# Performance work log

Hardware: AMD Instinct MI355X
Metric: run time of the kernel (lower is better)

## Reference

```python
import jax, jax.numpy as jnp
import numpy as np

H = 32          # query heads
KV = 8          # kv heads
DH = 64         # head dim
WINDOW = 1024   # sliding window
BASE = 10000.0  # rope base


def _rope(x, pos):
    """Interleaved RoPE as in RotaryEmbedding.apply. x: (B,H,T,Dh), pos: (T,)."""
    inv = 1.0 / (BASE ** (jnp.arange(0, DH, 2, dtype=jnp.float32) / DH))  # (Dh/2,)
    freqs = pos.astype(jnp.float32)[:, None] * inv[None, :]               # (T, Dh/2)
    cos = jnp.cos(freqs)[None, None].astype(x.dtype)
    sin = jnp.sin(freqs)[None, None].astype(x.dtype)
    x1, x2 = x[..., ::2], x[..., 1::2]
    o1 = x1 * cos - x2 * sin
    o2 = x1 * sin + x2 * cos
    return jnp.stack([o1, o2], axis=-1).reshape(x.shape)


def setup_inputs() -> dict:
    key = jax.random.key(0)
    ks = jax.random.split(key, 5)
    B, T, D, Tc = 2, 4096, 2048, 4096
    x = jax.random.normal(ks[0], (B, T, D), jnp.float32)
    k_cache = jax.random.normal(ks[1], (B, KV, Tc, DH), jnp.float32)
    v_cache = jax.random.normal(ks[2], (B, KV, Tc, DH), jnp.float32)
    Wq = jax.random.normal(ks[3], (D, D), jnp.float32) * 0.02
    Wo = jax.random.normal(ks[4], (D, D), jnp.float32) * 0.02
    return {"x": x, "k_cache": k_cache, "v_cache": v_cache, "Wq": Wq, "Wo": Wo}


def reference(x, k_cache, v_cache, Wq, Wo):
    """AttnLayer.forward, role='follower', local=True, return_attn=False, eval mode."""
    B, T, D = x.shape
    rep = H // KV
    # q projection: nn.Linear(d, H*Dh, bias=False) -> x @ W.T
    q = (x @ Wq.T).reshape(B, T, H, DH).transpose(0, 2, 1, 3)  # (B,H,T,Dh)
    Tc = k_cache.shape[2]
    pos_q = jnp.arange(Tc - T, Tc)
    q = _rope(q, pos_q)
    # GQA: KV -> H head replication (repeat_interleave along head dim)
    k = jnp.repeat(k_cache, rep, axis=1)  # (B,H,Tc,Dh)
    v = jnp.repeat(v_cache, rep, axis=1)
    # sliding-window slice: keep last `window` keys
    w = min(WINDOW, Tc)
    k = k[:, :, Tc - w:, :]  # (B,H,Tk,Dh)
    v = v[:, :, Tc - w:, :]
    Tk = w
    scale = 1.0 / np.sqrt(DH).astype(np.float32)
    scores = jnp.einsum('bhtd,bhsd->bhts', q, k) * scale  # (B,H,T,Tk)
    # torch SDPA is_causal with L != S uses a TOP-LEFT aligned tril mask: j <= i
    causal = jnp.arange(Tk)[None, :] <= jnp.arange(T)[:, None]  # (T,Tk)
    scores = jnp.where(causal[None, None], scores, -jnp.inf)
    attn = jax.nn.softmax(scores, axis=-1)
    out = jnp.einsum('bhts,bhsd->bhtd', attn, v)
    out = out.transpose(0, 2, 1, 3).reshape(B, T, H * DH)
    return out @ Wo.T
```

## Files before the change

### kernel.cpp

```cpp
#include <hip/hip_runtime.h>
#include <math.h>

typedef __attribute__((ext_vector_type(8))) short short8;
typedef __attribute__((ext_vector_type(4))) float floatx4;
typedef __attribute__((ext_vector_type(4))) unsigned int uintx4;
typedef __attribute__((ext_vector_type(2))) unsigned int uintx2;

#define MFMA16(a, b, c) __builtin_amdgcn_mfma_f32_16x16x32_bf16((a), (b), (c), 0, 0, 0)

#define QSCALE 0.18033688011112042f

__device__ __forceinline__ unsigned short f2bf(float x) {
    unsigned int u = __float_as_uint(x);
    u += 0x7fffu + ((u >> 16) & 1u);
    return (unsigned short)(u >> 16);
}

__device__ __forceinline__ short8 lds8(const unsigned short* p) {
    return *reinterpret_cast<const short8*>(p);
}

__device__ __forceinline__ void g2l16(const unsigned short* g, unsigned short* l) {
    __builtin_amdgcn_global_load_lds(
        (const __attribute__((address_space(1))) unsigned int*)g,
        (__attribute__((address_space(3))) unsigned int*)l,
        16, 0, 0);
}

__device__ __forceinline__ unsigned int cvtpk(float a, float b) {
    unsigned int r;
    asm("v_cvt_pk_bf16_f32 %0, %1, %2" : "=v"(r) : "v"(a), "v"(b));
    return r;
}

__device__ __forceinline__ void pl32swap(unsigned int& a, unsigned int& b) {
    asm("v_permlane32_swap_b32 %0, %1" : "+v"(a), "+v"(b));
}

__device__ __forceinline__ void pl16swap(unsigned int& a, unsigned int& b) {
    asm("v_permlane16_swap_b32 %0, %1" : "+v"(a), "+v"(b));
}

__global__ void cvt_bf16(const float* __restrict__ src, unsigned short* __restrict__ dst, int n4) {
    int i = blockIdx.x * blockDim.x + threadIdx.x;
    if (i >= n4) return;
    float4 v = reinterpret_cast<const float4*>(src)[i];
    ushort4 o;
    o.x = f2bf(v.x); o.y = f2bf(v.y); o.z = f2bf(v.z); o.w = f2bf(v.w);
    reinterpret_cast<ushort4*>(dst)[i] = o;
}

__global__ void prep_k(const float* __restrict__ kc, unsigned short* __restrict__ Kw) {
    int i = blockIdx.x * blockDim.x + threadIdx.x;
    int d4  = (i & 15) * 4;
    int s   = (i >> 4) & 1023;
    int bkv = i >> 14;
    size_t src = ((size_t)bkv * 4096 + 3072 + s) * 64 + d4;
    float4 kv = *reinterpret_cast<const float4*>(kc + src);
    ushort4 ko;
    ko.x = f2bf(kv.x); ko.y = f2bf(kv.y); ko.z = f2bf(kv.z); ko.w = f2bf(kv.w);
    *reinterpret_cast<ushort4*>(Kw + ((size_t)bkv * 1024 + s) * 64 + d4) = ko;
}

__global__ void prep_v(const float* __restrict__ vc, unsigned short* __restrict__ Vt) {
    __shared__ unsigned short tl[64][72];
    const int bkv = blockIdx.x >> 4;
    const int s0  = (blockIdx.x & 15) * 64;
    const int t   = threadIdx.x;
    const int sl  = t >> 2;
    const int dq  = (t & 3) * 16;
    const float* src = vc + ((size_t)bkv * 4096 + 3072 + s0 + sl) * 64 + dq;
    float4 v0 = reinterpret_cast<const float4*>(src)[0];
    float4 v1 = reinterpret_cast<const float4*>(src)[1];
    float4 v2 = reinterpret_cast<const float4*>(src)[2];
    float4 v3 = reinterpret_cast<const float4*>(src)[3];
    tl[dq +  0][sl] = f2bf(v0.x); tl[dq +  1][sl] = f2bf(v0.y);
    tl[dq +  2][sl] = f2bf(v0.z); tl[dq +  3][sl] = f2bf(v0.w);
    tl[dq +  4][sl] = f2bf(v1.x); tl[dq +  5][sl] = f2bf(v1.y);
    tl[dq +  6][sl] = f2bf(v1.z); tl[dq +  7][sl] = f2bf(v1.w);
    tl[dq +  8][sl] = f2bf(v2.x); tl[dq +  9][sl] = f2bf(v2.y);
    tl[dq + 10][sl] = f2bf(v2.z); tl[dq + 11][sl] = f2bf(v2.w);
    tl[dq + 12][sl] = f2bf(v3.x); tl[dq + 13][sl] = f2bf(v3.y);
    tl[dq + 14][sl] = f2bf(v3.z); tl[dq + 15][sl] = f2bf(v3.w);
    __syncthreads();
    const int dl = t >> 2;
    const int sc = (t & 3) * 16;
    unsigned short* dst = Vt + ((size_t)bkv * 64 + dl) * 1024 + s0 + sc;
    short8 x0 = *reinterpret_cast<const short8*>(&tl[dl][sc]);
    short8 x1 = *reinterpret_cast<const short8*>(&tl[dl][sc + 8]);
    *reinterpret_cast<short8*>(dst)     = x0;
    *reinterpret_cast<short8*>(dst + 8) = x1;
}

template <int EPI>
__global__ __launch_bounds__(256)
void gemm_bt(const unsigned short* __restrict__ A,
             const unsigned short* __restrict__ Bt,
             float* __restrict__ Cf,
             unsigned short* __restrict__ Cb) {
    constexpr int K = 2048;
    __shared__ unsigned short As[128 * 32];
    __shared__ unsigned short Bs[128 * 32];
    __shared__ float2 tab[EPI == 0 ? 128 * 33 : 1];

    const int tid  = threadIdx.x;
    const int lane = tid & 63;
    const int l15  = lane & 15;
    const int quad = lane >> 4;
    const int wid  = tid >> 6;
    const int wm   = (wid & 1) * 64;
    const int wn   = (wid >> 1) * 64;

    const int bn = blockIdx.x & 15;
    const int bm = blockIdx.x >> 4;

    if (EPI == 0) {
        const int t0 = (bm & 31) * 128;
        for (int e = tid; e < 4096; e += 256) {
            int tl = e >> 5, d2 = e & 31;
            float f = (float)(t0 + tl) * exp2f(-(float)d2 * 0.41524101186092f);
            float sn, cs; __sincosf(f, &sn, &cs);
            tab[tl * 33 + d2] = make_float2(cs, sn);
        }
    }

    const int row0 = tid >> 2;
    const int kc8  = (tid & 3) * 8;
    const unsigned short* Ag0 = A  + (size_t)(bm * 128 + row0) * K + kc8;
    const unsigned short* Ag1 = Ag0 + (size_t)64 * K;
    const unsigned short* Bg0 = Bt + (size_t)(bn * 128 + row0) * K + kc8;
    const unsigned short* Bg1 = Bg0 + (size_t)64 * K;
    unsigned short* AsW0 = As + wid * 512;
    unsigned short* AsW1 = As + 2048 + wid * 512;
    unsigned short* BsW0 = Bs + wid * 512;
    unsigned short* BsW1 = Bs + 2048 + wid * 512;

    floatx4 c00 = {0,0,0,0}, c01 = {0,0,0,0}, c02 = {0,0,0,0}, c03 = {0,0,0,0};
    floatx4 c10 = {0,0,0,0}, c11 = {0,0,0,0}, c12 = {0,0,0,0}, c13 = {0,0,0,0};
    floatx4 c20 = {0,0,0,0}, c21 = {0,0,0,0}, c22 = {0,0,0,0}, c23 = {0,0,0,0};
    floatx4 c30 = {0,0,0,0}, c31 = {0,0,0,0}, c32 = {0,0,0,0}, c33 = {0,0,0,0};

    for (int k0 = 0; k0 < K; k0 += 32) {
        __syncthreads();
        g2l16(Ag0 + k0, AsW0);
        g2l16(Ag1 + k0, AsW1);
        g2l16(Bg0 + k0, BsW0);
        g2l16(Bg1 + k0, BsW1);
        __syncthreads();

        short8 a0 = lds8(&As[(wm +  0 + l15) * 32 + quad * 8]);
        short8 a1 = lds8(&As[(wm + 16 + l15) * 32 + quad * 8]);
        short8 a2 = lds8(&As[(wm + 32 + l15) * 32 + quad * 8]);
        short8 a3 = lds8(&As[(wm + 48 + l15) * 32 + quad * 8]);
        short8 b0 = lds8(&Bs[(wn +  0 + l15) * 32 + quad * 8]);
        short8 b1 = lds8(&Bs[(wn + 16 + l15) * 32 + quad * 8]);
        short8 b2 = lds8(&Bs[(wn + 32 + l15) * 32 + quad * 8]);
        short8 b3 = lds8(&Bs[(wn + 48 + l15) * 32 + quad * 8]);

        c00 = MFMA16(a0, b0, c00); c01 = MFMA16(a0, b1, c01);
        c02 = MFMA16(a0, b2, c02); c03 = MFMA16(a0, b3, c03);
        c10 = MFMA16(a1, b0, c10); c11 = MFMA16(a1, b1, c11);
        c12 = MFMA16(a1, b2, c12); c13 = MFMA16(a1, b3, c13);
        c20 = MFMA16(a2, b0, c20); c21 = MFMA16(a2, b1, c21);
        c22 = MFMA16(a2, b2, c22); c23 = MFMA16(a2, b3, c23);
        c30 = MFMA16(a3, b0, c30); c31 = MFMA16(a3, b1, c31);
        c32 = MFMA16(a3, b2, c32); c33 = MFMA16(a3, b3, c33);
    }

#define EPI_TILE(i, j, C) do {                                                  \
    _Pragma("unroll")                                                           \
    for (int r = 0; r < 4; ++r) {                                               \
        int row = bm * 128 + wm + (i) * 16 + quad * 4 + r;                      \
        int col = bn * 128 + wn + (j) * 16 + l15;                               \
        float v = (C)[r];                                                       \
        if (EPI == 0) {                                                         \
            float p = __shfl_xor(v, 1);                                         \
            int t = row & 4095, b = row >> 12;                                  \
            int hh = col >> 6, d = col & 63;                                    \
            int tl = wm + (i) * 16 + quad * 4 + r;                              \
            float2 cspair = tab[tl * 33 + (d >> 1)];                            \
            float o = (d & 1) ? (p * cspair.y + v * cspair.x)                   \
                              : (v * cspair.x - p * cspair.y);                  \
            o *= QSCALE;                                                        \
            float po = __shfl_xor(o, 1);                                        \
            if (!(lane & 1)) {                                                  \
                unsigned int pk = (unsigned int)f2bf(o) |                       \
                                  ((unsigned int)f2bf(po) << 16);               \
                *reinterpret_cast<unsigned int*>(                               \
                    Cb + ((size_t)((b * 32 + hh) * 4096 + t)) * 64 + d) = pk;   \
            }                                                                   \
        } else {                                                                \
            Cf[(size_t)row * 2048 + col] = v;                                   \
        }                                                                       \
    }                                                                           \
} while (0)

    EPI_TILE(0, 0, c00); EPI_TILE(0, 1, c01); EPI_TILE(0, 2, c02); EPI_TILE(0, 3, c03);
    EPI_TILE(1, 0, c10); EPI_TILE(1, 1, c11); EPI_TILE(1, 2, c12); EPI_TILE(1, 3, c13);
    EPI_TILE(2, 0, c20); EPI_TILE(2, 1, c21); EPI_TILE(2, 2, c22); EPI_TILE(2, 3, c23);
    EPI_TILE(3, 0, c30); EPI_TILE(3, 1, c31); EPI_TILE(3, 2, c32); EPI_TILE(3, 3, c33);
#undef EPI_TILE
}

__global__ __launch_bounds__(256, 5)
void attn(const unsigned short* __restrict__ Q,
          const unsigned short* __restrict__ Kw,
          const unsigned short* __restrict__ Vt,
          unsigned short* __restrict__ O) {
    const int blk   = blockIdx.x;
    const int qtile = blk & 63;
    const int bh    = blk >> 6;
    const int h     = bh & 31;
    const int b     = bh >> 5;
    const int kvh   = h >> 2;

    const int tid  = threadIdx.x;
    const int lane = tid & 63;
    const int l15  = lane & 15;
    const int quad = lane >> 4;
    const int wid  = tid >> 6;
    const int qt0  = qtile * 64 + wid * 16;

    const unsigned short* Qp = Q  + ((size_t)bh * 4096 + qt0) * 64;
    const unsigned short* Kp = Kw + (size_t)(b * 8 + kvh) * 1024 * 64;
    const unsigned short* Vp = Vt + (size_t)(b * 8 + kvh) * 64 * 1024;

    __shared__ unsigned short Ks[2][4096];
    __shared__ unsigned short Vs[2][4096];

    short8 qa0 = lds8(&Qp[l15 * 64 + quad * 8]);
    short8 qa1 = lds8(&Qp[l15 * 64 + 32 + quad * 8]);

    const unsigned short* gK = Kp + (size_t)(wid * 16 + l15) * 64 + quad * 8;
    const unsigned short* gV = Vp + (size_t)(wid * 16 + l15) * 1024 + quad * 8;

    const int ntiles = (qtile < 15 ? qtile + 1 : 16);
    const int nkW    = (qt0 + 16 < 1024) ? qt0 + 16 : 1024;
    const bool diag  = (qtile < 16);

    g2l16(gK,      &Ks[0][wid * 1024]);
    g2l16(gK + 32, &Ks[0][wid * 1024 + 512]);
    g2l16(gV,      &Vs[0][wid * 1024]);
    g2l16(gV + 32, &Vs[0][wid * 1024 + 512]);

    floatx4 o0 = {0,0,0,0}, o1 = {0,0,0,0}, o2 = {0,0,0,0}, o3 = {0,0,0,0};
    float Lq = 0.f;
    float m = -INFINITY;

    for (int it = 0; it < ntiles; ++it) {
        __syncthreads();
        const int cur = it & 1;
        if (it + 1 < ntiles) {
            const int nxt = cur ^ 1;
            const unsigned short* gKn = gK + (it + 1) * 4096;
            const unsigned short* gVn = gV + (it + 1) * 64;
            g2l16(gKn,      &Ks[nxt][wid * 1024]);
            g2l16(gKn + 32, &Ks[nxt][wid * 1024 + 512]);
            g2l16(gVn,      &Vs[nxt][wid * 1024]);
            g2l16(gVn + 32, &Vs[nxt][wid * 1024 + 512]);
        }
        const int s0 = it << 6;
        const unsigned short* Kc = Ks[cur];
        const unsigned short* Vc = Vs[cur];

        floatx4 sS[4];
#pragma unroll
        for (int c = 0; c < 4; ++c) {
            floatx4 z = {0, 0, 0, 0};
            z = MFMA16(lds8(Kc + c * 1024 + lane * 8), qa0, z);
            z = MFMA16(lds8(Kc + c * 1024 + 512 + lane * 8), qa1, z);
            sS[c] = z;
        }

        const bool last = (it == ntiles - 1);
        bool skipHi = false;
        if (last && diag) {
#pragma unroll
            for (int c = 0; c < 4; ++c)
#pragma unroll
                for (int r = 0; r < 4; ++r)
                    if (s0 + c * 16 + quad * 4 + r > qt0 + l15) sS[c][r] = -INFINITY;
            skipHi = (nkW - s0 <= 32);
        }

        float t0 = fmaxf(fmaxf(sS[0][0], sS[0][1]), fmaxf(sS[0][2], sS[0][3]));
        float t1 = fmaxf(fmaxf(sS[1][0], sS[1][1]), fmaxf(sS[1][2], sS[1][3]));
        float t2 = fmaxf(fmaxf(sS[2][0], sS[2][1]), fmaxf(sS[2][2], sS[2][3]));
        float t3 = fmaxf(fmaxf(sS[3][0], sS[3][1]), fmaxf(sS[3][2], sS[3][3]));
        float mx = fmaxf(fmaxf(t0, t1), fmaxf(t2, t3));
        mx = fmaxf(mx, __shfl_xor(mx, 16));
        mx = fmaxf(mx, __shfl_xor(mx, 32));

        if (!__all(mx <= m + 8.0f)) {
            const float mn = fmaxf(m, mx);
            const float alpha = exp2f(m - mn);
            m = mn;
            o0 *= alpha; o1 *= alpha; o2 *= alpha; o3 *= alpha;
            Lq *= alpha;
        }

        float p[4][4];
#pragma unroll
        for (int c = 0; c < 4; ++c)
#pragma unroll
            for (int r = 0; r < 4; ++r) p[c][r] = exp2f(sS[c][r] - m);
        Lq += ((p[0][0] + p[0][1] + p[0][2] + p[0][3]) + (p[1][0] + p[1][1] + p[1][2] + p[1][3]))
            + ((p[2][0] + p[2][1] + p[2][2] + p[2][3]) + (p[3][0] + p[3][1] + p[3][2] + p[3][3]));

        unsigned int a0 = cvtpk(p[0][0], p[0][1]);
        unsigned int a1 = cvtpk(p[0][2], p[0][3]);
        unsigned int a2 = cvtpk(p[1][0], p[1][1]);
        unsigned int a3 = cvtpk(p[1][2], p[1][3]);
        pl32swap(a0, a2); pl32swap(a1, a3);
        pl16swap(a0, a2); pl16swap(a1, a3);
        uintx4 tlo = {a0, a1, a2, a3};
        short8 pa_lo = __builtin_bit_cast(short8, tlo);

        o0 = MFMA16(lds8(Vc + 0 * 512 + lane * 8), pa_lo, o0);
        o1 = MFMA16(lds8(Vc + 2 * 512 + lane * 8), pa_lo, o1);
        o2 = MFMA16(lds8(Vc + 4 * 512 + lane * 8), pa_lo, o2);
        o3 = MFMA16(lds8(Vc + 6 * 512 + lane * 8), pa_lo, o3);
        if (!skipHi) {
            unsigned int b0 = cvtpk(p[2][0], p[2][1]);
            unsigned int b1 = cvtpk(p[2][2], p[2][3]);
            unsigned int b2 = cvtpk(p[3][0], p[3][1]);
            unsigned int b3 = cvtpk(p[3][2], p[3][3]);
            pl32swap(b0, b2); pl32swap(b1, b3);
            pl16swap(b0, b2); pl16swap(b1, b3);
            uintx4 thi = {b0, b1, b2, b3};
            short8 pa_hi = __builtin_bit_cast(short8, thi);
            o0 = MFMA16(lds8(Vc + 1 * 512 + lane * 8), pa_hi, o0);
            o1 = MFMA16(lds8(Vc + 3 * 512 + lane * 8), pa_hi, o1);
            o2 = MFMA16(lds8(Vc + 5 * 512 + lane * 8), pa_hi, o2);
            o3 = MFMA16(lds8(Vc + 7 * 512 + lane * 8), pa_hi, o3);
        }
    }

    Lq += __shfl_xor(Lq, 16);
    Lq += __shfl_xor(Lq, 32);
    const float inv = 1.f / Lq;

    unsigned short* Op = O + (size_t)b * 4096 * 2048 + (size_t)(qt0 + l15) * 2048
                           + h * 64 + quad * 4;
    uintx2 w0, w1, w2, w3;
    w0.x = cvtpk(o0[0] * inv, o0[1] * inv); w0.y = cvtpk(o0[2] * inv, o0[3] * inv);
    w1.x = cvtpk(o1[0] * inv, o1[1] * inv); w1.y = cvtpk(o1[2] * inv, o1[3] * inv);
    w2.x = cvtpk(o2[0] * inv, o2[1] * inv); w2.y = cvtpk(o2[2] * inv, o2[3] * inv);
    w3.x = cvtpk(o3[0] * inv, o3[1] * inv); w3.y = cvtpk(o3[2] * inv, o3[3] * inv);
    *reinterpret_cast<uintx2*>(Op)      = w0;
    *reinterpret_cast<uintx2*>(Op + 16) = w1;
    *reinterpret_cast<uintx2*>(Op + 32) = w2;
    *reinterpret_cast<uintx2*>(Op + 48) = w3;
}

extern "C" void kernel_launch(void* const* d_in, const int* in_sizes, int n_in,
                              void* d_out, int out_size, void* d_ws, size_t ws_size,
                              hipStream_t stream) {
    const float* x  = (const float*)d_in[0];
    const float* kc = (const float*)d_in[1];
    const float* vc = (const float*)d_in[2];
    const float* Wq = (const float*)d_in[3];
    const float* Wo = (const float*)d_in[4];
    float* out = (float*)d_out;

    char* ws = (char*)d_ws;
    unsigned short* Xb  = (unsigned short*)(ws);
    unsigned short* Qb  = (unsigned short*)(ws + 33554432);
    unsigned short* Wqb = (unsigned short*)(ws + 67108864);
    unsigned short* Wob = (unsigned short*)(ws + 75497472);
    unsigned short* Kwb = (unsigned short*)(ws + 83886080);
    unsigned short* Vtb = (unsigned short*)(ws + 85983232);

    cvt_bf16<<<16384, 256, 0, stream>>>(x,  Xb,  4194304);
    cvt_bf16<<<4096,  256, 0, stream>>>(Wq, Wqb, 1048576);
    cvt_bf16<<<4096,  256, 0, stream>>>(Wo, Wob, 1048576);
    prep_k<<<1024, 256, 0, stream>>>(kc, Kwb);
    prep_v<<<256, 256, 0, stream>>>(vc, Vtb);

    gemm_bt<0><<<1024, 256, 0, stream>>>(Xb, Wqb, nullptr, Qb);
    attn<<<4096, 256, 0, stream>>>(Qb, Kwb, Vtb, Xb);
    gemm_bt<1><<<1024, 256, 0, stream>>>(Xb, Wob, out, nullptr);
}
```

Measured before the change: 511.3 us.

## Use 8-wave attention blocks covering 128 queries to share K/V tiles

The attention kernel now launches half as many blocks, each with 512 threads covering 128 query rows instead of 64. Each K/V LDS tile is loaded cooperatively by eight waves, so every global K/V tile is fetched once per 128 queries rather than once per 64, which halves global and LDS fill traffic. Waves whose causal window ends early skip the compute for tiles beyond their own range but still take part in loading and barriers. The cost is some idle waves on diagonal blocks, and the launch bound of 512 threads at 8 waves per SIMD tightens the register budget.

```diff
diff --git a/kernel.cpp b/kernel.cpp
--- a/kernel.cpp
+++ b/kernel.cpp
@@ -202,24 +202,24 @@
 #undef EPI_TILE
 }
 
-__global__ __launch_bounds__(256, 5)
+__global__ __launch_bounds__(512, 8)
 void attn(const unsigned short* __restrict__ Q,
           const unsigned short* __restrict__ Kw,
           const unsigned short* __restrict__ Vt,
           unsigned short* __restrict__ O) {
-    const int blk   = blockIdx.x;
-    const int qtile = blk & 63;
-    const int bh    = blk >> 6;
-    const int h     = bh & 31;
-    const int b     = bh >> 5;
-    const int kvh   = h >> 2;
+    const int blk  = blockIdx.x;
+    const int qblk = blk & 31;
+    const int bh   = blk >> 5;
+    const int h    = bh & 31;
+    const int b    = bh >> 5;
+    const int kvh  = h >> 2;
 
     const int tid  = threadIdx.x;
     const int lane = tid & 63;
     const int l15  = lane & 15;
     const int quad = lane >> 4;
     const int wid  = tid >> 6;
-    const int qt0  = qtile * 64 + wid * 16;
+    const int qt0  = qblk * 128 + wid * 16;
 
     const unsigned short* Qp = Q  + ((size_t)bh * 4096 + qt0) * 64;
     const unsigned short* Kp = Kw + (size_t)(b * 8 + kvh) * 1024 * 64;
@@ -231,17 +231,22 @@
     short8 qa0 = lds8(&Qp[l15 * 64 + quad * 8]);
     short8 qa1 = lds8(&Qp[l15 * 64 + 32 + quad * 8]);
 
-    const unsigned short* gK = Kp + (size_t)(wid * 16 + l15) * 64 + quad * 8;
-    const unsigned short* gV = Vp + (size_t)(wid * 16 + l15) * 1024 + quad * 8;
-
-    const int ntiles = (qtile < 15 ? qtile + 1 : 16);
+    const unsigned short* gK = Kp + (size_t)((wid >> 1) * 16 + l15) * 64
+                                  + (wid & 1) * 32 + quad * 8;
+    const unsigned short* gV = Vp + (size_t)((wid >> 1) * 16 + l15) * 1024
+                                  + (wid & 1) * 32 + quad * 8;
+    unsigned short* sK0 = &Ks[0][wid * 512];
+    unsigned short* sK1 = &Ks[1][wid * 512];
+    unsigned short* sV0 = &Vs[0][wid * 512];
+    unsigned short* sV1 = &Vs[1][wid * 512];
+
+    const int ntiles = (qblk < 7 ? 2 * qblk + 2 : 16);
     const int nkW    = (qt0 + 16 < 1024) ? qt0 + 16 : 1024;
-    const bool diag  = (qtile < 16);
-
-    g2l16(gK,      &Ks[0][wid * 1024]);
-    g2l16(gK + 32, &Ks[0][wid * 1024 + 512]);
-    g2l16(gV,      &Vs[0][wid * 1024]);
-    g2l16(gV + 32, &Vs[0][wid * 1024 + 512]);
+    const int ntW    = (nkW + 63) >> 6;
+    const bool diagW = (qt0 < 1024);
+
+    g2l16(gK, sK0);
+    g2l16(gV, sV0);
 
     floatx4 o0 = {0,0,0,0}, o1 = {0,0,0,0}, o2 = {0,0,0,0}, o3 = {0,0,0,0};
     float Lq = 0.f;
@@ -251,14 +256,10 @@
         __syncthreads();
         const int cur = it & 1;
         if (it + 1 < ntiles) {
-            const int nxt = cur ^ 1;
-            const unsigned short* gKn = gK + (it + 1) * 4096;
-            const unsigned short* gVn = gV + (it + 1) * 64;
-            g2l16(gKn,      &Ks[nxt][wid * 1024]);
-            g2l16(gKn + 32, &Ks[nxt][wid * 1024 + 512]);
-            g2l16(gVn,      &Vs[nxt][wid * 1024]);
-            g2l16(gVn + 32, &Vs[nxt][wid * 1024 + 512]);
-        }
+            g2l16(gK + (it + 1) * 4096, cur ? sK0 : sK1);
+            g2l16(gV + (it + 1) * 64,   cur ? sV0 : sV1);
+        }
+        if (it >= ntW) continue;
         const int s0 = it << 6;
         const unsigned short* Kc = Ks[cur];
         const unsigned short* Vc = Vs[cur];
@@ -272,9 +273,9 @@
             sS[c] = z;
         }
 
-        const bool last = (it == ntiles - 1);
+        const bool last = (it == ntW - 1);
         bool skipHi = false;
-        if (last && diag) {
+        if (last && diagW) {
 #pragma unroll
             for (int c = 0; c < 4; ++c)
 #pragma unroll
@@ -378,6 +379,6 @@
     prep_v<<<256, 256, 0, stream>>>(vc, Vtb);
 
     gemm_bt<0><<<1024, 256, 0, stream>>>(Xb, Wqb, nullptr, Qb);
-    attn<<<4096, 256, 0, stream>>>(Qb, Kwb, Vtb, Xb);
+    attn<<<2048, 512, 0, stream>>>(Qb, Kwb, Vtb, Xb);
     gemm_bt<1><<<1024, 256, 0, stream>>>(Xb, Wob, out, nullptr);
 }
```

New measurement: 505.8 us. Within noise of the previous version (-1.1%).
